# Performance work log

Measured on AMD Instinct MI355X. Metric: run time of the kernel, lower is better.

The kernel has to match this reference:

```python
import jax, jax.numpy as jnp
import numpy as np

B, N, D = 8, 8192, 512
H, WIDTH = 8, 2048
DH = D // H
EPS = 1e-5


def _ln(x, g, b):
    m = jnp.mean(x, axis=-1, keepdims=True)
    v = jnp.mean(jnp.square(x - m), axis=-1, keepdims=True)
    return (x - m) * jax.lax.rsqrt(v + EPS) * g + b


def setup_inputs() -> dict:
    key = jax.random.key(0)
    ks = jax.random.split(key, 16)
    s = 0.02
    return {
        "x": jax.random.normal(ks[0], (B, N, D), dtype=jnp.float32),
        "mask": jnp.ones((B, N), dtype=jnp.float32),
        "Wq": jax.random.normal(ks[1], (D, D), dtype=jnp.float32) * s,
        "bq": jnp.zeros((D,), dtype=jnp.float32),
        "Wk": jax.random.normal(ks[2], (D, D), dtype=jnp.float32) * s,
        "bk": jnp.zeros((D,), dtype=jnp.float32),
        "Wv": jax.random.normal(ks[3], (D, D), dtype=jnp.float32) * s,
        "bv": jnp.zeros((D,), dtype=jnp.float32),
        "q_alpha": jax.random.normal(ks[4], (H, DH), dtype=jnp.float32),
        "k_beta": jax.random.normal(ks[5], (H, DH), dtype=jnp.float32),
        "Wo": jax.random.normal(ks[6], (D, D), dtype=jnp.float32) * s,
        "bo": jnp.zeros((D,), dtype=jnp.float32),
        "ln0_g": jnp.ones((D,), dtype=jnp.float32),
        "ln0_b": jnp.zeros((D,), dtype=jnp.float32),
        "ln1_g": jnp.ones((D,), dtype=jnp.float32),
        "ln1_b": jnp.zeros((D,), dtype=jnp.float32),
        "W1": jax.random.normal(ks[7], (WIDTH, D), dtype=jnp.float32) * s,
        "b1": jnp.zeros((WIDTH,), dtype=jnp.float32),
        "W2": jax.random.normal(ks[8], (D, WIDTH), dtype=jnp.float32) * s,
        "b2": jnp.zeros((D,), dtype=jnp.float32),
    }


def reference(x, mask, Wq, bq, Wk, bk, Wv, bv, q_alpha, k_beta, Wo, bo,
              ln0_g, ln0_b, ln1_g, ln1_b, W1, b1, W2, b2):
    scale = DH ** -0.5
    mask_ = mask[..., None]                       # [B,N,1]
    valid = (mask != 0)[..., None]                # [B,N,1] bool, broadcast over H

    residual = x
    xn = _ln(x, ln0_g, ln0_b) * mask_

    Q = (xn @ Wq.T + bq).reshape(B, N, H, DH)
    K = (xn @ Wk.T + bk).reshape(B, N, H, DH)
    V = (xn @ Wv.T + bv).reshape(B, N, H, DH)

    # stage 1: global query pooling
    alpha = jnp.einsum('bnhd,hd->bnh', Q, q_alpha) * scale
    alpha = jnp.where(valid, alpha, -jnp.inf)
    alpha = jax.nn.softmax(alpha, axis=1)         # softmax over N
    global_q = jnp.einsum('bnhd,bnh->bhd', Q, alpha)

    # stage 2: global value pooling
    P = K * global_q[:, None]                     # [B,N,H,DH]
    beta = jnp.einsum('bnhd,hd->bnh', P, k_beta) * scale
    beta = jnp.where(valid, beta, -jnp.inf)
    beta = jax.nn.softmax(beta, axis=1)
    global_v = jnp.einsum('bnhd,bnh->bhd', V, beta)

    out = (Q + global_v[:, None]).reshape(B, N, D)
    out = out @ Wo.T + bo
    x = residual + out

    residual = x
    xn = _ln(x, ln1_g, ln1_b)
    h = jax.nn.gelu(xn @ W1.T + b1, approximate=False)
    h = jax.nn.gelu(h @ W2.T + b2, approximate=False)
    x = residual + h
    x = x * mask_
    return x
```

## Files before the change

kernel.cpp:

```cpp
#include <hip/hip_runtime.h>
#include <hip/hip_bf16.h>
#include <math.h>

typedef short s8v __attribute__((ext_vector_type(8)));
typedef short s4v __attribute__((ext_vector_type(4)));
typedef __bf16 bf8v __attribute__((ext_vector_type(8)));
typedef float f4v __attribute__((ext_vector_type(4)));

#define GLOBAL_AS __attribute__((address_space(1)))
#define LDS_AS __attribute__((address_space(3)))

static __device__ __forceinline__ float bf2f(ushort u) {
  return __builtin_bit_cast(float, (unsigned int)u << 16);
}
static __device__ __forceinline__ ushort f2bf(float f) {
  unsigned int u = __builtin_bit_cast(unsigned int, f);
  u += 0x7FFFu + ((u >> 16) & 1u);
  return (ushort)(u >> 16);
}
static __device__ __forceinline__ float gelu_f(float v) {
  float t = v * v;
  float u = v * (0.0356774081f * t + 0.7978845608f);
  float e = __expf(-2.0f * u);
  return v * __builtin_amdgcn_rcpf(1.0f + e);
}
static __device__ __forceinline__ float wave_max_f(float v) {
  #pragma unroll
  for (int o = 32; o >= 1; o >>= 1) v = fmaxf(v, __shfl_xor(v, o));
  return v;
}
static __device__ __forceinline__ float wave_sum_f(float v) {
  #pragma unroll
  for (int o = 32; o >= 1; o >>= 1) v += __shfl_xor(v, o);
  return v;
}
static __device__ __forceinline__ void gload16(const ushort* g, const ushort* l) {
  __builtin_amdgcn_global_load_lds(
      (const GLOBAL_AS unsigned int*)g,
      (LDS_AS unsigned int*)l, 16, 0, 0);
}

__global__ void cvt_f32_bf16(const float* __restrict__ in, ushort* __restrict__ out, int n) {
  int i = (blockIdx.x * 256 + threadIdx.x) * 4;
  if (i >= n) return;
  float4 v = *(const float4*)(in + i);
  s4v o;
  o[0] = (short)f2bf(v.x); o[1] = (short)f2bf(v.y);
  o[2] = (short)f2bf(v.z); o[3] = (short)f2bf(v.w);
  *(s4v*)(out + i) = o;
}

__global__ __launch_bounds__(256) void transpose512(
    const float* __restrict__ in, float* __restrict__ out) {
  __shared__ float t[32][33];
  const int bx = blockIdx.x & 15, by = blockIdx.x >> 4;
  const int tx = threadIdx.x & 31, ty = threadIdx.x >> 5;
  #pragma unroll
  for (int i = 0; i < 4; ++i)
    t[ty + i * 8][tx] = in[(long)(by * 32 + ty + i * 8) * 512 + bx * 32 + tx];
  __syncthreads();
  #pragma unroll
  for (int i = 0; i < 4; ++i)
    out[(long)(bx * 32 + ty + i * 8) * 512 + by * 32 + tx] = t[tx][ty + i * 8];
}

__global__ __launch_bounds__(256) void wqo_kernel(
    const float* __restrict__ Wo, const float* __restrict__ Wq,
    ushort* __restrict__ WqoB)
{
  __shared__ float lO[64][33];
  __shared__ float lQ[32][65];
  const int t = threadIdx.x;
  const int bi = (blockIdx.x & 7) * 64, bj = (blockIdx.x >> 3) * 64;
  float acc[16] = {};
  for (int k0 = 0; k0 < 512; k0 += 32) {
    __syncthreads();
    {
      const int r = t >> 2, c = (t & 3) * 8;
      #pragma unroll
      for (int j = 0; j < 8; ++j) lO[r][c + j] = Wo[(long)(bi + r) * 512 + k0 + c + j];
      const int r2 = t >> 3, c2 = (t & 7) * 8;
      #pragma unroll
      for (int j = 0; j < 8; ++j) lQ[r2][c2 + j] = Wq[(long)(k0 + r2) * 512 + bj + c2 + j];
    }
    __syncthreads();
    const int j = t & 63, ig = t >> 6;
    for (int kk = 0; kk < 32; ++kk) {
      float q = lQ[kk][j];
      #pragma unroll
      for (int ii = 0; ii < 16; ++ii) acc[ii] += lO[ig * 16 + ii][kk] * q;
    }
  }
  const int j = t & 63, ig = t >> 6;
  #pragma unroll
  for (int ii = 0; ii < 16; ++ii)
    WqoB[(long)(bi + ig * 16 + ii) * 512 + bj + j] = f2bf(acc[ii]);
}

__global__ __launch_bounds__(256) void wa_kernel(
    const float* __restrict__ qa, const float* __restrict__ Wq,
    const float* __restrict__ bqv, ushort* __restrict__ waB, float* __restrict__ ca)
{
  __shared__ float ql[64];
  const int h = blockIdx.x;
  const int t = threadIdx.x;
  if (h >= 8) {
    waB[h * 512 + t] = 0; waB[h * 512 + 256 + t] = 0;
    if (t == 0) ca[h] = 0.f;
    return;
  }
  if (t < 64) ql[t] = qa[h * 64 + t];
  __syncthreads();
  #pragma unroll
  for (int half = 0; half < 2; ++half) {
    const int k = half * 256 + t;
    float s = 0;
    for (int dd = 0; dd < 64; ++dd) s += ql[dd] * Wq[(long)(h * 64 + dd) * 512 + k];
    waB[h * 512 + k] = f2bf(s);
  }
  if (t == 0) {
    float s = 0;
    for (int dd = 0; dd < 64; ++dd) s += ql[dd] * bqv[h * 64 + dd];
    ca[h] = s;
  }
}

__global__ __launch_bounds__(256) void ln_rows(
    const float* __restrict__ x, const float* __restrict__ gam,
    const float* __restrict__ bet, const float* __restrict__ mask,
    ushort* __restrict__ out)
{
  const int tid = threadIdx.x, lane = tid & 63, wv = tid >> 6;
  const long row = (long)blockIdx.x * 4 + wv;
  const float* xp = x + row * 512 + lane * 8;
  float4 a = *(const float4*)xp;
  float4 b = *(const float4*)(xp + 4);
  float s = a.x + a.y + a.z + a.w + b.x + b.y + b.z + b.w;
  float q = a.x*a.x + a.y*a.y + a.z*a.z + a.w*a.w
          + b.x*b.x + b.y*b.y + b.z*b.z + b.w*b.w;
  s = wave_sum_f(s); q = wave_sum_f(q);
  float m = s * (1.f / 512.f);
  float var = q * (1.f / 512.f) - m * m;
  float r = rsqrtf(var + 1e-5f);
  float mk = mask ? mask[row] : 1.f;
  const float* gp = gam + lane * 8;
  const float* bp = bet + lane * 8;
  float4 g0 = *(const float4*)gp, g1 = *(const float4*)(gp + 4);
  float4 c0 = *(const float4*)bp, c1 = *(const float4*)(bp + 4);
  s8v o;
  o[0] = (short)f2bf(((a.x - m) * r * g0.x + c0.x) * mk);
  o[1] = (short)f2bf(((a.y - m) * r * g0.y + c0.y) * mk);
  o[2] = (short)f2bf(((a.z - m) * r * g0.z + c0.z) * mk);
  o[3] = (short)f2bf(((a.w - m) * r * g0.w + c0.w) * mk);
  o[4] = (short)f2bf(((b.x - m) * r * g1.x + c1.x) * mk);
  o[5] = (short)f2bf(((b.y - m) * r * g1.y + c1.y) * mk);
  o[6] = (short)f2bf(((b.z - m) * r * g1.z + c1.z) * mk);
  o[7] = (short)f2bf(((b.w - m) * r * g1.w + c1.w) * mk);
  *(s8v*)(out + row * 512 + lane * 8) = o;
}

__global__ __launch_bounds__(256) void ln_rows_bf16(
    const ushort* __restrict__ x, const float* __restrict__ gam,
    const float* __restrict__ bet, ushort* __restrict__ out)
{
  const int tid = threadIdx.x, lane = tid & 63, wv = tid >> 6;
  const long row = (long)blockIdx.x * 4 + wv;
  s8v v = *(const s8v*)(x + row * 512 + lane * 8);
  float xv[8];
  #pragma unroll
  for (int j = 0; j < 8; ++j) xv[j] = bf2f((ushort)v[j]);
  float s = 0.f, q = 0.f;
  #pragma unroll
  for (int j = 0; j < 8; ++j) { s += xv[j]; q += xv[j] * xv[j]; }
  s = wave_sum_f(s); q = wave_sum_f(q);
  float m = s * (1.f / 512.f);
  float var = q * (1.f / 512.f) - m * m;
  float r = rsqrtf(var + 1e-5f);
  const float* gp = gam + lane * 8;
  const float* bp = bet + lane * 8;
  float4 g0 = *(const float4*)gp, g1 = *(const float4*)(gp + 4);
  float4 c0 = *(const float4*)bp, c1 = *(const float4*)(bp + 4);
  float gg[8] = {g0.x, g0.y, g0.z, g0.w, g1.x, g1.y, g1.z, g1.w};
  float cc[8] = {c0.x, c0.y, c0.z, c0.w, c1.x, c1.y, c1.z, c1.w};
  s8v o;
  #pragma unroll
  for (int j = 0; j < 8; ++j) o[j] = (short)f2bf((xv[j] - m) * r * gg[j] + cc[j]);
  *(s8v*)(out + row * 512 + lane * 8) = o;
}

template<int BS, int CS>
__global__ __launch_bounds__(256) void logits_k(
    const ushort* __restrict__ XN, const ushort* __restrict__ Wl,
    const float* __restrict__ cvec, const float* __restrict__ mask,
    float* __restrict__ outL)
{
  __shared__ ushort lw[16 * 512];
  const int tid = threadIdx.x, lane = tid & 63, wv = tid >> 6;
  const long r0 = (long)blockIdx.x * 64;
  const int b = (int)(r0 >> 13);
  #pragma unroll
  for (int i = 0; i < 4; ++i) {
    const int u = tid + i * 256;
    const int h2 = u >> 6, uu = u & 63;
    s8v v = *(const s8v*)(Wl + (long)b * BS + h2 * 512 + uu * 8);
    *(s8v*)(lw + h2 * 512 + (uu ^ (h2 & 7)) * 8) = v;
  }
  __syncthreads();
  const int h = lane & 15, q = lane >> 4;
  const long rw = r0 + wv * 16;
  const ushort* ap = XN + (rw + (lane & 15)) * 512 + q * 8;
  f4v acc = {};
  #pragma unroll
  for (int t = 0; t < 16; ++t) {
    bf8v a = *(const bf8v*)(ap + t * 32);
    bf8v bb = *(const bf8v*)(lw + h * 512 + (((t * 4 + q) ^ (h & 7))) * 8);
    acc = __builtin_amdgcn_mfma_f32_16x16x32_bf16(a, bb, acc, 0, 0, 0);
  }
  const float cv = cvec[b * CS + h];
  #pragma unroll
  for (int j = 0; j < 4; ++j) {
    const long n = rw + q * 4 + j;
    float v = (acc[j] + cv) * 0.125f;
    if (mask[n] == 0.f) v = -1e30f;
    if (h < 8) outL[((long)((b << 3) + h) << 13) + (n & 8191)] = v;
  }
}

__global__ __launch_bounds__(1024) void softmax_rows(float* __restrict__ L)
{
  __shared__ float red[16];
  __shared__ float bc;
  const int tid = threadIdx.x, lane = tid & 63, wv = tid >> 6;
  float* p = L + ((long)blockIdx.x << 13) + tid * 8;
  float4 v0 = *(float4*)p;
  float4 v1 = *(float4*)(p + 4);
  float m = fmaxf(fmaxf(fmaxf(v0.x, v0.y), fmaxf(v0.z, v0.w)),
                  fmaxf(fmaxf(v1.x, v1.y), fmaxf(v1.z, v1.w)));
  m = wave_max_f(m);
  if (lane == 0) red[wv] = m;
  __syncthreads();
  if (tid < 64) {
    float t = (lane < 16) ? red[lane] : -INFINITY;
    t = wave_max_f(t);
    if (lane == 0) bc = t;
  }
  __syncthreads();
  const float gm = bc;
  v0.x = __expf(v0.x - gm); v0.y = __expf(v0.y - gm);
  v0.z = __expf(v0.z - gm); v0.w = __expf(v0.w - gm);
  v1.x = __expf(v1.x - gm); v1.y = __expf(v1.y - gm);
  v1.z = __expf(v1.z - gm); v1.w = __expf(v1.w - gm);
  float s = v0.x + v0.y + v0.z + v0.w + v1.x + v1.y + v1.z + v1.w;
  s = wave_sum_f(s);
  __syncthreads();
  if (lane == 0) red[wv] = s;
  __syncthreads();
  if (tid < 64) {
    float t = (lane < 16) ? red[lane] : 0.f;
    t = wave_sum_f(t);
    if (lane == 0) bc = t;
  }
  __syncthreads();
  const float inv = 1.0f / bc;
  v0.x *= inv; v0.y *= inv; v0.z *= inv; v0.w *= inv;
  v1.x *= inv; v1.y *= inv; v1.z *= inv; v1.w *= inv;
  *(float4*)p = v0;
  *(float4*)(p + 4) = v1;
}

__global__ __launch_bounds__(256) void pool_w(
    const ushort* __restrict__ XN, const float* __restrict__ wbuf,
    float* __restrict__ part)
{
  __shared__ float wlds[128][8];
  __shared__ float cmb[4][512];
  const int tid = threadIdx.x;
  const int b = blockIdx.x >> 6, ch = blockIdx.x & 63;
  const long g0 = ((long)b << 13) + ch * 128;
  if (tid < 128) {
    #pragma unroll
    for (int h = 0; h < 8; ++h)
      wlds[tid][h] = wbuf[(((long)(b * 8 + h)) << 13) + ch * 128 + tid];
  }
  __syncthreads();
  const int rg = tid >> 6, c8 = (tid & 63) * 8;
  f4v acc[8][2] = {};
  for (int it = 0; it < 32; ++it) {
    const int r = it * 4 + rg;
    s8v xv = *(const s8v*)(XN + (g0 + r) * 512 + c8);
    float xf[8];
    #pragma unroll
    for (int j = 0; j < 8; ++j) xf[j] = bf2f((ushort)xv[j]);
    #pragma unroll
    for (int h = 0; h < 8; ++h) {
      const float w = wlds[r][h];
      #pragma unroll
      for (int j = 0; j < 8; ++j) acc[h][j >> 2][j & 3] += w * xf[j];
    }
  }
  #pragma unroll
  for (int h = 0; h < 8; ++h) {
    __syncthreads();
    #pragma unroll
    for (int j = 0; j < 8; ++j) cmb[rg][c8 + j] = acc[h][j >> 2][j & 3];
    __syncthreads();
    const int col = tid * 2;
    float s0 = cmb[0][col] + cmb[1][col] + cmb[2][col] + cmb[3][col];
    float s1 = cmb[0][col + 1] + cmb[1][col + 1] + cmb[2][col + 1] + cmb[3][col + 1];
    *(float2*)(part + (((long)blockIdx.x * 8 + h) << 9) + col) = make_float2(s0, s1);
  }
}

__global__ __launch_bounds__(256) void combine_px(
    const float* __restrict__ part, float* __restrict__ px)
{
  const int bh = blockIdx.x;
  const int b = bh >> 3, h = bh & 7;
  const int col = threadIdx.x * 2;
  float s0 = 0.f, s1 = 0.f;
  for (int ch = 0; ch < 64; ++ch) {
    const float* p = part + (((long)((b * 64 + ch) * 8 + h)) << 9) + col;
    s0 += p[0]; s1 += p[1];
  }
  px[(bh << 9) + col] = s0;
  px[(bh << 9) + col + 1] = s1;
}

__global__ __launch_bounds__(64) void prep_gq_wb(
    const float* __restrict__ px, const float* __restrict__ WqT,
    const float* __restrict__ bqv, const float* __restrict__ kbv,
    const float* __restrict__ Wk, const float* __restrict__ bkv,
    ushort* __restrict__ wbB, float* __restrict__ cbs)
{
  __shared__ float pxl[512];
  __shared__ float gkb[64];
  const int bh = blockIdx.x, b = bh >> 3, h = bh & 7, d = threadIdx.x;
  #pragma unroll
  for (int i = 0; i < 8; ++i) pxl[d + i * 64] = px[(bh << 9) + d + i * 64];
  __syncthreads();
  float acc = bqv[h * 64 + d];
  for (int c = 0; c < 512; ++c) acc += pxl[c] * WqT[(long)c * 512 + h * 64 + d];
  gkb[d] = acc * kbv[h * 64 + d];
  __syncthreads();
  float s[8] = {};
  for (int dd = 0; dd < 64; ++dd) {
    const float g = gkb[dd];
    const float* wr = Wk + (long)(h * 64 + dd) * 512 + d;
    #pragma unroll
    for (int ki = 0; ki < 8; ++ki) s[ki] += g * wr[ki * 64];
  }
  #pragma unroll
  for (int ki = 0; ki < 8; ++ki)
    wbB[(long)(b * 16 + h) * 512 + d + ki * 64] = f2bf(s[ki]);
  if (d == 0) {
    float t = 0.f;
    for (int dd = 0; dd < 64; ++dd) t += gkb[dd] * bkv[h * 64 + dd];
    cbs[b * 16 + h] = t;
  }
  if (h == 0) {
    #pragma unroll
    for (int hp = 8; hp < 16; ++hp)
      for (int k = d; k < 512; k += 64) wbB[(long)(b * 16 + hp) * 512 + k] = 0;
    if (d < 8) cbs[b * 16 + 8 + d] = 0.f;
  }
}

__global__ __launch_bounds__(64) void prep_gv(
    const float* __restrict__ pv, const float* __restrict__ WvT,
    const float* __restrict__ bvv, const float* __restrict__ bqv,
    float* __restrict__ gvb)
{
  __shared__ float pxl[512];
  const int bh = blockIdx.x, b = bh >> 3, h = bh & 7, d = threadIdx.x;
  #pragma unroll
  for (int i = 0; i < 8; ++i) pxl[d + i * 64] = pv[(bh << 9) + d + i * 64];
  __syncthreads();
  float acc = bvv[h * 64 + d] + bqv[h * 64 + d];
  for (int c = 0; c < 512; ++c) acc += pxl[c] * WvT[(long)c * 512 + h * 64 + d];
  gvb[b * 512 + h * 64 + d] = acc;
}

__global__ __launch_bounds__(256) void bias_gv(
    const float* __restrict__ gv, const float* __restrict__ Wo,
    const float* __restrict__ bo, float* __restrict__ bo2) {
  const int b = blockIdx.x;
  const int n = blockIdx.y * 256 + threadIdx.x;
  const float* g = gv + b * 512;
  const float* w = Wo + (long)n * 512;
  float acc = 0.f;
  for (int d = 0; d < 512; d += 4) {
    float4 wv4 = *(const float4*)(w + d);
    acc += g[d] * wv4.x + g[d + 1] * wv4.y + g[d + 2] * wv4.z + g[d + 3] * wv4.w;
  }
  bo2[b * 512 + n] = bo[n] + acc;
}

#define MFMA_(d,a,b) d = __builtin_amdgcn_mfma_f32_16x16x32_bf16(a, b, d, 0, 0, 0)

template<int EPI, int LDA, int NN, int KK>
__global__ __launch_bounds__(512, 4) void gemmP(
    const ushort* __restrict__ A, const ushort* __restrict__ W,
    const float* __restrict__ bias, const void* __restrict__ resid,
    const float* __restrict__ mask, void* __restrict__ Out)
{
  constexpr int NBX = NN / 256;
  constexpr int NT = KK / 32;
  __shared__ __align__(16) ushort lds[3][12288];
  const int tid = threadIdx.x;
  const int lane = tid & 63;
  const int w = tid >> 6;
  const int wm = w >> 2, wn = w & 3;

  const int nwg = gridDim.x;
  const int cpx = nwg >> 3;
  const int wg = (blockIdx.x & 7) * cpx + (blockIdx.x >> 3);
  const int bx = wg % NBX, by = wg / NBX;
  const long bm = (long)by * 128;
  const int bn = bx * 256;

  const int scr = tid >> 2, sls = tid & 3;
  const int akU = ((sls ^ (scr & 3) ^ ((scr >> 2) & 3))) * 8;
  const ushort* asrc = A + (bm + scr) * (long)LDA + akU;
  const int rbe = (scr & 31) + ((scr >> 5) << 6);
  const ushort* besrc = W + (long)(bn + rbe) * KK + akU;
  const ushort* bosrc = W + (long)(bn + rbe + 32) * KK + akU;

#define STG(b_, Tt) { \
    gload16(asrc + (Tt) * 32, &lds[b_][tid * 8]); \
    gload16(besrc + (Tt) * 32, &lds[b_][4096 + tid * 8]); \
    gload16(bosrc + (Tt) * 32, &lds[b_][8192 + tid * 8]); }

  STG(0, 0);
  STG(1, 1);

  f4v acc[4][4] = {};

  const int L = lane & 15, q = lane >> 4;
  const int soff = (q ^ (lane & 3) ^ ((lane >> 2) & 3)) * 8;
  const int abase = (wm * 64 + L) * 32 + soff;
  const int bbase = 4096 + (wn * 32 + L) * 32 + soff;

  asm volatile("s_waitcnt vmcnt(3)" ::: "memory");
  asm volatile("s_barrier" ::: "memory");

  for (int T = 0; T < NT; ++T) {
    const ushort* Lp = &lds[T % 3][0];
    bf8v aR[4], bR[4];
    #pragma unroll
    for (int m = 0; m < 4; ++m) aR[m] = *(const bf8v*)(Lp + abase + m * 512);
    bR[0] = *(const bf8v*)(Lp + bbase);
    bR[1] = *(const bf8v*)(Lp + bbase + 512);
    bR[2] = *(const bf8v*)(Lp + bbase + 4096);
    bR[3] = *(const bf8v*)(Lp + bbase + 4096 + 512);
    if (T + 2 < NT) {
      STG((T + 2) % 3, T + 2);
      asm volatile("s_waitcnt vmcnt(3)" ::: "memory");
    } else {
      asm volatile("s_waitcnt vmcnt(0)" ::: "memory");
    }
    asm volatile("s_barrier" ::: "memory");
    __builtin_amdgcn_s_setprio(1);
    #pragma unroll
    for (int m = 0; m < 4; ++m)
      #pragma unroll
      for (int n = 0; n < 4; ++n)
        MFMA_(acc[m][n], aR[m], bR[n]);
    __builtin_amdgcn_s_setprio(0);
  }
#undef STG

  const int colb = bn + wn * 64 + L;
  const long rowb = bm + wm * 64 + q * 4;
  const float* biasp = (EPI == 5) ? bias + ((bm >> 13) << 9) : bias;
  #pragma unroll
  for (int m = 0; m < 4; ++m) {
    #pragma unroll
    for (int j = 0; j < 4; ++j) {
      const long row = rowb + m * 16 + j;
      #pragma unroll
      for (int n = 0; n < 4; ++n) {
        const int col = colb + n * 16;
        float v = acc[m][n][j] + biasp[col];
        const long idx = row * (long)NN + col;
        if constexpr (EPI == 2) {
          ((ushort*)Out)[idx] = f2bf(gelu_f(v));
        } else if constexpr (EPI == 3) {
          ((float*)Out)[idx] = (bf2f(((const ushort*)resid)[idx]) + gelu_f(v)) * mask[row];
        } else {
          ((ushort*)Out)[idx] = f2bf(v + ((const float*)resid)[idx]);
        }
      }
    }
  }
}

extern "C" void kernel_launch(void* const* d_in, const int* in_sizes, int n_in,
                              void* d_out, int out_size, void* d_ws, size_t ws_size,
                              hipStream_t stream) {
  const float* x    = (const float*)d_in[0];
  const float* mask = (const float*)d_in[1];
  const float* Wq   = (const float*)d_in[2];
  const float* bq   = (const float*)d_in[3];
  const float* Wk   = (const float*)d_in[4];
  const float* bk   = (const float*)d_in[5];
  const float* Wv   = (const float*)d_in[6];
  const float* bv   = (const float*)d_in[7];
  const float* qa   = (const float*)d_in[8];
  const float* kb   = (const float*)d_in[9];
  const float* Wo   = (const float*)d_in[10];
  const float* bo   = (const float*)d_in[11];
  const float* g0   = (const float*)d_in[12];
  const float* be0  = (const float*)d_in[13];
  const float* g1   = (const float*)d_in[14];
  const float* be1  = (const float*)d_in[15];
  const float* W1   = (const float*)d_in[16];
  const float* b1   = (const float*)d_in[17];
  const float* W2   = (const float*)d_in[18];
  const float* b2   = (const float*)d_in[19];
  float* out = (float*)d_out;

  const int M = 65536;
  char* ws = (char*)d_ws;
  const size_t MB = 1024 * 1024;
  ushort* XN  = (ushort*)(ws);
  ushort* X1  = (ushort*)(ws + 64 * MB);
  ushort* H1  = (ushort*)(ws + 192 * MB);
  float*  AL  = (float*)(ws + 192 * MB);
  float*  BL  = (float*)(ws + 194 * MB);
  float*  PART= (float*)(ws + 196 * MB);
  char* base = ws + 448 * MB;
  ushort* W1B  = (ushort*)(base);
  ushort* W2B  = (ushort*)(base + 2 * MB);
  ushort* WqoB = (ushort*)(base + 4 * MB);
  float*  WqT  = (float*)(base + 4 * MB + 512 * 1024);
  float*  WvT  = (float*)(base + 5 * MB + 512 * 1024);
  ushort* waB  = (ushort*)(base + 6 * MB + 512 * 1024);
  ushort* wbB  = (ushort*)(base + 6 * MB + 528 * 1024);
  float*  ca   = (float*)(base + 6 * MB + 656 * 1024);
  float*  cbs  = (float*)(base + 6 * MB + 660 * 1024);
  float*  PX   = (float*)(base + 6 * MB + 664 * 1024);
  float*  PV   = (float*)(base + 6 * MB + 792 * 1024);
  float*  GVB  = (float*)(base + 6 * MB + 920 * 1024);
  float*  BO2  = (float*)(base + 6 * MB + 936 * 1024);

  cvt_f32_bf16<<<1024, 256, 0, stream>>>(W1, W1B, 1048576);
  cvt_f32_bf16<<<1024, 256, 0, stream>>>(W2, W2B, 1048576);
  wqo_kernel<<<64, 256, 0, stream>>>(Wo, Wq, WqoB);
  wa_kernel<<<16, 256, 0, stream>>>(qa, Wq, bq, waB, ca);
  transpose512<<<256, 256, 0, stream>>>(Wq, WqT);
  transpose512<<<256, 256, 0, stream>>>(Wv, WvT);

  ln_rows<<<M / 4, 256, 0, stream>>>(x, g0, be0, mask, XN);

  logits_k<0, 0><<<1024, 256, 0, stream>>>(XN, waB, ca, mask, AL);
  softmax_rows<<<64, 1024, 0, stream>>>(AL);
  pool_w<<<512, 256, 0, stream>>>(XN, AL, PART);
  combine_px<<<64, 256, 0, stream>>>(PART, PX);
  prep_gq_wb<<<64, 64, 0, stream>>>(PX, WqT, bq, kb, Wk, bk, wbB, cbs);

  logits_k<8192, 16><<<1024, 256, 0, stream>>>(XN, wbB, cbs, mask, BL);
  softmax_rows<<<64, 1024, 0, stream>>>(BL);
  pool_w<<<512, 256, 0, stream>>>(XN, BL, PART);
  combine_px<<<64, 256, 0, stream>>>(PART, PV);
  prep_gv<<<64, 64, 0, stream>>>(PV, WvT, bv, bq, GVB);
  bias_gv<<<dim3(8, 2), 256, 0, stream>>>(GVB, Wo, bo, BO2);

  gemmP<5, 512, 512, 512><<<2 * (M / 128), 512, 0, stream>>>(
      XN, WqoB, BO2, x, nullptr, X1);

  ln_rows_bf16<<<M / 4, 256, 0, stream>>>(X1, g1, be1, XN);

  gemmP<2, 512, 2048, 512><<<8 * (M / 128), 512, 0, stream>>>(
      XN, W1B, b1, nullptr, nullptr, H1);
  gemmP<3, 2048, 512, 2048><<<2 * (M / 128), 512, 0, stream>>>(
      H1, W2B, b2, X1, mask, out);
}
```

Measured before the change: 712.9 us.

## Use FP8 for the second MLP GEMM with a dedicated FP8 MFMA kernel

The first MLP GEMM now writes its GELU output as FP8 e4m3 instead of bf16, and W2 is converted to FP8. A new gemmF8 kernel runs the 2048-deep second MLP GEMM with fp8 MFMA instructions, staging A and W tiles into LDS with a triple-buffered pipeline. This halves the bytes of the H1 intermediate and the W2 weights and uses the higher-throughput FP8 matrix path. It costs precision in the hidden activations and weights, which may affect accuracy tolerance.

```diff
diff --git a/kernel.cpp b/kernel.cpp
--- a/kernel.cpp
+++ b/kernel.cpp
@@ -1,5 +1,6 @@
 #include <hip/hip_runtime.h>
 #include <hip/hip_bf16.h>
+#include <hip/hip_fp8.h>
 #include <math.h>
 
 typedef short s8v __attribute__((ext_vector_type(8)));
@@ -17,6 +18,15 @@
   unsigned int u = __builtin_bit_cast(unsigned int, f);
   u += 0x7FFFu + ((u >> 16) & 1u);
   return (ushort)(u >> 16);
+}
+static __device__ __forceinline__ unsigned char f2fp8(float f) {
+#if __has_builtin(__builtin_amdgcn_cvt_pk_fp8_f32)
+  int p = __builtin_amdgcn_cvt_pk_fp8_f32(f, f, 0, false);
+  return (unsigned char)(p & 0xFF);
+#else
+  __hip_fp8_e4m3 v(f);
+  return (unsigned char)v.__x;
+#endif
 }
 static __device__ __forceinline__ float gelu_f(float v) {
   float t = v * v;
@@ -34,7 +44,7 @@
   for (int o = 32; o >= 1; o >>= 1) v += __shfl_xor(v, o);
   return v;
 }
-static __device__ __forceinline__ void gload16(const ushort* g, const ushort* l) {
+static __device__ __forceinline__ void gload16(const void* g, const void* l) {
   __builtin_amdgcn_global_load_lds(
       (const GLOBAL_AS unsigned int*)g,
       (LDS_AS unsigned int*)l, 16, 0, 0);
@@ -48,6 +58,15 @@
   o[0] = (short)f2bf(v.x); o[1] = (short)f2bf(v.y);
   o[2] = (short)f2bf(v.z); o[3] = (short)f2bf(v.w);
   *(s4v*)(out + i) = o;
+}
+
+__global__ void cvt_f32_fp8(const float* __restrict__ in, unsigned char* __restrict__ out, int n) {
+  int i = (blockIdx.x * 256 + threadIdx.x) * 4;
+  if (i >= n) return;
+  float4 v = *(const float4*)(in + i);
+  uchar4 o;
+  o.x = f2fp8(v.x); o.y = f2fp8(v.y); o.z = f2fp8(v.z); o.w = f2fp8(v.w);
+  *(uchar4*)(out + i) = o;
 }
 
 __global__ __launch_bounds__(256) void transpose512(
@@ -482,13 +501,110 @@
         const int col = colb + n * 16;
         float v = acc[m][n][j] + biasp[col];
         const long idx = row * (long)NN + col;
-        if constexpr (EPI == 2) {
-          ((ushort*)Out)[idx] = f2bf(gelu_f(v));
-        } else if constexpr (EPI == 3) {
-          ((float*)Out)[idx] = (bf2f(((const ushort*)resid)[idx]) + gelu_f(v)) * mask[row];
+        if constexpr (EPI == 6) {
+          ((unsigned char*)Out)[idx] = f2fp8(gelu_f(v));
         } else {
           ((ushort*)Out)[idx] = f2bf(v + ((const float*)resid)[idx]);
         }
+      }
+    }
+  }
+}
+
+__global__ __launch_bounds__(512, 4) void gemmF8(
+    const unsigned char* __restrict__ A, const unsigned char* __restrict__ W,
+    const float* __restrict__ bias, const ushort* __restrict__ resid,
+    const float* __restrict__ mask, float* __restrict__ Out)
+{
+  constexpr int NN = 512, KK = 2048;
+  constexpr int NBX = 2;
+  constexpr int NT = KK / 64;
+  __shared__ __align__(16) unsigned char lds8[3][24576];
+  const int tid = threadIdx.x;
+  const int lane = tid & 63;
+  const int w = tid >> 6;
+  const int wm = w >> 2, wn = w & 3;
+
+  const int nwg = gridDim.x;
+  const int cpx = nwg >> 3;
+  const int wg = (blockIdx.x & 7) * cpx + (blockIdx.x >> 3);
+  const int bx = wg % NBX, by = wg / NBX;
+  const long bm = (long)by * 128;
+  const int bn = bx * 256;
+
+  const int srow = tid >> 2;
+  const int sxu = (tid & 3) ^ ((srow >> 1) & 3);
+  const unsigned char* asrc = A + (bm + srow) * (long)KK + sxu * 16;
+  const unsigned char* b0src = W + (long)(bn + srow) * KK + sxu * 16;
+  const unsigned char* b1src = W + (long)(bn + srow + 128) * KK + sxu * 16;
+
+#define STG8(b_, Tt) { \
+    gload16(asrc + (Tt) * 64, &lds8[b_][tid * 16]); \
+    gload16(b0src + (Tt) * 64, &lds8[b_][8192 + tid * 16]); \
+    gload16(b1src + (Tt) * 64, &lds8[b_][16384 + tid * 16]); }
+
+  STG8(0, 0);
+  STG8(1, 1);
+
+  f4v acc[4][4] = {};
+
+  const int L = lane & 15, q = lane >> 4;
+  const int s0 = ((q) ^ (L & 6)) * 8;
+  const int s1 = ((4 + q) ^ (L & 6)) * 8;
+  const int arow = (wm * 64 + L) * 64;
+  const int brow = 8192 + (wn * 64 + L) * 64;
+
+  asm volatile("s_waitcnt vmcnt(3)" ::: "memory");
+  asm volatile("s_barrier" ::: "memory");
+
+  for (int T = 0; T < NT; ++T) {
+    const unsigned char* Lp = &lds8[T % 3][0];
+    long aF[8], bF[8];
+    #pragma unroll
+    for (int m = 0; m < 4; ++m) {
+      aF[2 * m]     = *(const long*)(Lp + arow + m * 1024 + s0);
+      aF[2 * m + 1] = *(const long*)(Lp + arow + m * 1024 + s1);
+    }
+    #pragma unroll
+    for (int n = 0; n < 4; ++n) {
+      bF[2 * n]     = *(const long*)(Lp + brow + n * 1024 + s0);
+      bF[2 * n + 1] = *(const long*)(Lp + brow + n * 1024 + s1);
+    }
+    if (T + 2 < NT) {
+      STG8((T + 2) % 3, T + 2);
+      asm volatile("s_waitcnt vmcnt(3)" ::: "memory");
+    } else {
+      asm volatile("s_waitcnt vmcnt(0)" ::: "memory");
+    }
+    asm volatile("s_barrier" ::: "memory");
+    __builtin_amdgcn_s_setprio(1);
+    #pragma unroll
+    for (int m = 0; m < 4; ++m)
+      #pragma unroll
+      for (int n = 0; n < 4; ++n) {
+        acc[m][n] = __builtin_amdgcn_mfma_f32_16x16x32_fp8_fp8(
+            aF[2 * m], bF[2 * n], acc[m][n], 0, 0, 0);
+        acc[m][n] = __builtin_amdgcn_mfma_f32_16x16x32_fp8_fp8(
+            aF[2 * m + 1], bF[2 * n + 1], acc[m][n], 0, 0, 0);
+      }
+    __builtin_amdgcn_s_setprio(0);
+  }
+#undef STG8
+
+  const int colb = bn + wn * 64 + L;
+  const long rowb = bm + wm * 64 + q * 4;
+  #pragma unroll
+  for (int m = 0; m < 4; ++m) {
+    #pragma unroll
+    for (int j = 0; j < 4; ++j) {
+      const long row = rowb + m * 16 + j;
+      const float mk = mask[row];
+      #pragma unroll
+      for (int n = 0; n < 4; ++n) {
+        const int col = colb + n * 16;
+        float v = acc[m][n][j] + bias[col];
+        const long idx = row * (long)NN + col;
+        Out[idx] = (bf2f(resid[idx]) + gelu_f(v)) * mk;
       }
     }
   }
@@ -524,13 +640,13 @@
   const size_t MB = 1024 * 1024;
   ushort* XN  = (ushort*)(ws);
   ushort* X1  = (ushort*)(ws + 64 * MB);
-  ushort* H1  = (ushort*)(ws + 192 * MB);
+  unsigned char* H1F = (unsigned char*)(ws + 192 * MB);
   float*  AL  = (float*)(ws + 192 * MB);
   float*  BL  = (float*)(ws + 194 * MB);
   float*  PART= (float*)(ws + 196 * MB);
   char* base = ws + 448 * MB;
   ushort* W1B  = (ushort*)(base);
-  ushort* W2B  = (ushort*)(base + 2 * MB);
+  unsigned char* W2F = (unsigned char*)(base + 2 * MB);
   ushort* WqoB = (ushort*)(base + 4 * MB);
   float*  WqT  = (float*)(base + 4 * MB + 512 * 1024);
   float*  WvT  = (float*)(base + 5 * MB + 512 * 1024);
@@ -544,7 +660,7 @@
   float*  BO2  = (float*)(base + 6 * MB + 936 * 1024);
 
   cvt_f32_bf16<<<1024, 256, 0, stream>>>(W1, W1B, 1048576);
-  cvt_f32_bf16<<<1024, 256, 0, stream>>>(W2, W2B, 1048576);
+  cvt_f32_fp8<<<1024, 256, 0, stream>>>(W2, W2F, 1048576);
   wqo_kernel<<<64, 256, 0, stream>>>(Wo, Wq, WqoB);
   wa_kernel<<<16, 256, 0, stream>>>(qa, Wq, bq, waB, ca);
   transpose512<<<256, 256, 0, stream>>>(Wq, WqT);
@@ -570,8 +686,8 @@
 
   ln_rows_bf16<<<M / 4, 256, 0, stream>>>(X1, g1, be1, XN);
 
-  gemmP<2, 512, 2048, 512><<<8 * (M / 128), 512, 0, stream>>>(
-      XN, W1B, b1, nullptr, nullptr, H1);
-  gemmP<3, 2048, 512, 2048><<<2 * (M / 128), 512, 0, stream>>>(
-      H1, W2B, b2, X1, mask, out);
-}
+  gemmP<6, 512, 2048, 512><<<8 * (M / 128), 512, 0, stream>>>(
+      XN, W1B, b1, nullptr, nullptr, H1F);
+  gemmF8<<<2 * (M / 128), 512, 0, stream>>>(
+      H1F, W2F, b2, X1, mask, out);
+}
```

After: 631.8 us. 1.13x faster.
